# Kernel optimization log

Hardware: AMD Instinct MI355X
Metric: run time of the kernel (lower is better)

Reference implementation:

```python
import jax, jax.numpy as jnp
import numpy as np
from jax import lax

CODEBOOK_DIM = 32
SCALE_SCHEDULE = [1, 2, 4, 8, 16, 32, 64, 128, 256, 512, 1024, 2048, 4096, 8192]
INV_TEMP = 100.0
COMMIT_W = 0.2
ENTROPY_W = 0.1
EPS_NORM = 1e-12
EPS_LOG = 1e-8


def setup_inputs() -> dict:
    key = jax.random.key(0)
    B, T, C = 32, 8192, CODEBOOK_DIM
    f_BTC = jax.random.normal(key, (B, T, C), dtype=jnp.float32)
    return {"f_BTC": f_BTC}


def _area_down(x, pt):
    # torch F.interpolate mode='area' on divisible sizes == average pooling
    B, T, C = x.shape
    if pt == T:
        return x
    return x.reshape(B, pt, T // pt, C).mean(axis=2)


def _linear_up(x, out_size):
    # torch F.interpolate mode='linear', align_corners=False
    B, in_size, C = x.shape
    if out_size == in_size:
        return x
    scale = in_size / out_size
    pos = (jnp.arange(out_size, dtype=jnp.float32) + 0.5) * scale - 0.5
    pos = jnp.clip(pos, 0.0, in_size - 1)
    lo = jnp.floor(pos).astype(jnp.int32)
    hi = jnp.minimum(lo + 1, in_size - 1)
    w = (pos - lo.astype(jnp.float32))[None, :, None]
    return x[:, lo] * (1.0 - w) + x[:, hi] * w


def _bsq_level(z):
    # normalize
    norm = jnp.sqrt(jnp.sum(z * z, axis=-1, keepdims=True))
    z = z / jnp.maximum(norm, EPS_NORM)
    q_scale = 1.0 / (CODEBOOK_DIM ** 0.5)
    zhat = jnp.where(z > 0, q_scale, -q_scale).astype(z.dtype)
    quant = z + lax.stop_gradient(zhat - z)  # STE
    # soft entropy loss
    p = jax.nn.sigmoid(-4.0 * z / (CODEBOOK_DIM ** 0.5) * INV_TEMP)
    ent = lambda c: -(c * jnp.log(c + EPS_LOG))
    per_sample = (ent(p) + ent(1.0 - p)).sum(axis=-1).mean()
    avg_p = p.mean(axis=(0, 1))  # [C]
    cb_ent = (ent(avg_p) + ent(1.0 - avg_p)).sum()
    entropy_penalty = (per_sample - cb_ent) / INV_TEMP
    commit = jnp.mean(((lax.stop_gradient(quant) - z) ** 2).sum(axis=-1))
    aux = entropy_penalty * ENTROPY_W + commit * COMMIT_W
    bits = (quant > 0).astype(jnp.int32)
    return quant, bits, aux


def reference(f_BTC):
    B, T, C = f_BTC.shape
    quantized_out = jnp.zeros_like(f_BTC)
    residual = f_BTC
    all_losses, all_bits = [], []
    for pt in SCALE_SCHEDULE:
        r = _area_down(residual, pt)
        quant, bits, loss = _bsq_level(r)
        q_up = _linear_up(quant, T)
        residual = residual - lax.stop_gradient(q_up)
        quantized_out = quantized_out + q_up
        all_bits.append(bits)
        all_losses.append(loss)
    return quantized_out, jnp.concatenate(all_bits, axis=1), jnp.stack(all_losses, axis=-1)
```

## Files before the change

### kernel.cpp

```cpp
#include <hip/hip_runtime.h>

#define B_DIM 32
#define T_DIM 8192
#define C_DIM 32
#define N_ELEM (B_DIM * T_DIM * C_DIM)
#define SUM_PT 16383
#define BITS_ELEM (B_DIM * SUM_PT * C_DIM)
#define NLEVEL 14
#define PARTB 8192
#define PARTS 512
#define QSCALE 0.17677669529663687f
#define ALPHA  70.710678118654755f

#define OWN 128
#define HALO 16
#define MAXL (OWN + 2 * HALO)

__device__ __forceinline__ float entf(float x) { return -(x * __logf(x + 1e-8f)); }
__device__ __forceinline__ float qval(float bit) { return bit * (2.0f * QSCALE) - QSCALE; }

__device__ __forceinline__ float interp_pk(const unsigned int* __restrict__ pkbase,
                                           int ptj, float tpos, int c) {
    const float a = (float)ptj * (1.0f / (float)T_DIM);
    float pos = (tpos + 0.5f) * a - 0.5f;
    pos = fminf(fmaxf(pos, 0.0f), (float)(ptj - 1));
    const int lo = (int)pos;
    const int hi = min(lo + 1, ptj - 1);
    const float w = pos - (float)lo;
    const float b0 = (float)((pkbase[lo] >> c) & 1u);
    const float b1 = (float)((pkbase[hi] >> c) & 1u);
    return ((b0 * (1.0f - w) + b1 * w) * 2.0f - 1.0f) * QSCALE;
}

template <int PTJ>
__device__ __forceinline__ float interp_loc(const unsigned int* __restrict__ bl,
                                            int p0, float tpos, int c) {
    const float a = (float)PTJ * (1.0f / (float)T_DIM);
    float pos = (tpos + 0.5f) * a - 0.5f;
    pos = fminf(fmaxf(pos, 0.0f), (float)(PTJ - 1));
    const int lo = (int)pos;
    const int hi = min(lo + 1, PTJ - 1);
    const float w = pos - (float)lo;
    const float b0 = (float)((bl[lo - p0] >> c) & 1u);
    const float b1 = (float)((bl[hi - p0] >> c) & 1u);
    return ((b0 * (1.0f - w) + b1 * w) * 2.0f - 1.0f) * QSCALE;
}

__device__ __forceinline__ float evalT(const unsigned int* __restrict__ bl,
                                       float w, int pk, int c) {
    const float b0 = (float)((bl[pk & 0xFFFF] >> c) & 1u);
    const float b1 = (float)((bl[pk >> 16] >> c) & 1u);
    return ((b0 * (1.0f - w) + b1 * w) * 2.0f - 1.0f) * QSCALE;
}

__device__ float pooled_up_sum64(const float* base, int ptj, int m) {
    const int W = 64;
    const float a = (float)ptj * (1.0f / (float)T_DIM);
    const float p0 = ((float)(m * W) + 0.5f) * a - 0.5f;
    const float pmax = (float)(ptj - 1);
    float sum = 0.0f;
    int iL = 0;
    if (p0 < 0.0f) { iL = (int)ceilf(-p0 / a); if (iL > W) iL = W; }
    int iH = W - 1;
    if (p0 + (float)(W - 1) * a > pmax) {
        iH = (int)floorf((pmax - p0) / a);
        if (iH > W - 1) iH = W - 1;
        if (iH < -1) iH = -1;
    }
    if (iL > 0) sum += (float)iL * qval(base[0]);
    if (iH < W - 1) sum += (float)(W - 1 - iH) * qval(base[(size_t)(ptj - 1) * C_DIM]);
    if (iH >= iL) {
        const float pL = p0 + (float)iL * a;
        int l0 = (int)pL;
        if (l0 > ptj - 1) l0 = ptj - 1;
        const int is = (int)ceilf(((float)(l0 + 1) - p0) / a);
        const int endA = min(is - 1, iH);
        if (endA >= iL) {
            const int nA = endA - iL + 1;
            const float sI = 0.5f * (float)(iL + endA) * (float)nA;
            const float SA = (float)nA * (p0 - (float)l0) + a * sI;
            const float q0 = qval(base[(size_t)l0 * C_DIM]);
            const float q1 = qval(base[(size_t)min(l0 + 1, ptj - 1) * C_DIM]);
            sum += (float)nA * q0 + SA * (q1 - q0);
        }
        const int begB = max(is, iL);
        if (begB <= iH) {
            const int nB = iH - begB + 1;
            const float sI = 0.5f * (float)(begB + iH) * (float)nB;
            const float SB = (float)nB * (p0 - (float)(l0 + 1)) + a * sI;
            const float q1 = qval(base[(size_t)min(l0 + 1, ptj - 1) * C_DIM]);
            const float q2 = qval(base[(size_t)min(l0 + 2, ptj - 1) * C_DIM]);
            sum += (float)nB * q1 + SB * (q2 - q1);
        }
    }
    return sum;
}

__device__ __forceinline__ void wave_partials(float e, float cm, float p,
                                              float* base, int stride, int col) {
    float eg = e, cg = cm;
#pragma unroll
    for (int m = 32; m >= 1; m >>= 1) { eg += __shfl_xor(eg, m, 64); cg += __shfl_xor(cg, m, 64); }
    const float p2 = p + __shfl_xor(p, 32, 64);
    const int lane = threadIdx.x & 63;
    if (lane < 32) base[(size_t)(2 + lane) * stride + col] = p2;
    if (lane == 0) { base[col] = eg; base[(size_t)stride + col] = cg; }
}

__device__ __forceinline__ float bsq_eval(float v, float& bit, float& pA, float& eA, float& cA) {
    float sq = v * v;
#pragma unroll
    for (int m = 16; m >= 1; m >>= 1) sq += __shfl_xor(sq, m, 32);
    const float z = v / fmaxf(sqrtf(sq), 1e-12f);
    bit = (z > 0.f) ? 1.0f : 0.0f;
    const float zh = (z > 0.f) ? QSCALE : -QSCALE;
    const float d = zh - z;
    cA += d * d;
    const float p = 1.0f / (1.0f + __expf(ALPHA * z));
    pA += p;
    eA += entf(p) + entf(1.0f - p);
    return zh;
}

__global__ void init_kernel(const float* __restrict__ f, float* __restrict__ F128) {
    const int b = blockIdx.x >> 7, m = blockIdx.x & 127;
    const int c = threadIdx.x & 31, grp = threadIdx.x >> 5;
    const float* fb = f + ((size_t)b * T_DIM + m * 64 + grp * 8) * C_DIM + c;
    float s = 0.f;
#pragma unroll
    for (int i = 0; i < 8; ++i) s += fb[i * C_DIM];
    __shared__ float red[8][32];
    red[grp][c] = s;
    __syncthreads();
    if (grp == 0) {
        float t = red[0][c] + red[1][c] + red[2][c] + red[3][c]
                + red[4][c] + red[5][c] + red[6][c] + red[7][c];
        F128[((size_t)b * 128 + m) * C_DIM + c] = t * (1.0f / 64.0f);
    }
}

__global__ __launch_bounds__(1024) void fused_small_kernel(const float* __restrict__ F128,
                                                           float* __restrict__ bits,
                                                           unsigned int* __restrict__ pkG,
                                                           float* __restrict__ pSm) {
    const int b = blockIdx.x;
    __shared__ float P[128 * 32];
    __shared__ float qh[127 * 32];
    const int c = threadIdx.x & 31, grp = threadIdx.x >> 5;
    const int col = b * 16 + (threadIdx.x >> 6);
    for (int i = threadIdx.x; i < 128 * 32; i += 1024) P[i] = F128[(size_t)b * 128 * 32 + i];
    __syncthreads();
    for (int k = 0; k < 8; ++k) {
        const int pt = 1 << k, W2 = 128 >> k;
        float pAcc = 0.f, eAcc = 0.f, cAcc = 0.f;
        for (int o = grp; o < pt; o += 32) {
            float v = 0.f;
            for (int i = 0; i < W2; ++i) v += P[(o * W2 + i) * 32 + c];
            v *= (1.0f / (float)W2);
            float bit;
            bsq_eval(v, bit, pAcc, eAcc, cAcc);
            bits[((size_t)b * SUM_PT + (pt - 1) + o) * C_DIM + c] = bit;
            const unsigned long long bal = __ballot(bit > 0.5f);
            if (c == 0)
                pkG[(size_t)b * 256 + (pt - 1) + o] =
                    (threadIdx.x & 32) ? (unsigned)(bal >> 32) : (unsigned)bal;
            if (k < 7) qh[((pt - 1) + o) * 32 + c] = bit;
        }
        wave_partials(eAcc, cAcc, pAcc, pSm + (size_t)k * 34 * PARTS, PARTS, col);
        if (k < 7) {
            __syncthreads();
            for (int m = grp; m < 128; m += 32)
                P[m * 32 + c] -= pooled_up_sum64(&qh[(pt - 1) * 32 + c], 1 << k, m) * (1.0f / 64.0f);
            __syncthreads();
        }
    }
}

template <int K, int J, int TO>
__device__ __forceinline__ void buildTab(float* tw, int* ti, int L0, int nL) {
    constexpr int FK = 4096 >> K;
    constexpr int ptj = 1 << J;
    constexpr int FJ = 4096 >> J;
    const int pN = nL / FK;
    const int p0j = L0 / FJ;
    const int pNj = nL / FJ;
    for (int pl = threadIdx.x; pl < pN; pl += 512) {
        const float tpos = (float)(2 * (L0 + pl * FK) + FK) - 0.5f;
        const float a = (float)ptj * (1.0f / (float)T_DIM);
        float pos = (tpos + 0.5f) * a - 0.5f;
        pos = fminf(fmaxf(pos, 0.0f), (float)(ptj - 1));
        const int lo = (int)pos;
        const int hi = min(lo + 1, ptj - 1);
        tw[TO + pl] = pos - (float)lo;
        const int lol = min(max(lo - p0j, 0), pNj - 1);
        const int hil = min(max(hi - p0j, 0), pNj - 1);
        ti[TO + pl] = lol | (hil << 16);
    }
}

template <int K>
__device__ __forceinline__ void cf_level(const float* Rl, unsigned int* bitsPyr,
                                         const float* tw, const int* ti,
                                         float* __restrict__ bits,
                                         float* __restrict__ pBig,
                                         int b, int L0, int nL, int r0, int r1,
                                         int c, int grp, int col) {
    constexpr int F = 4096 >> K;
    constexpr int ptk = 1 << K;
    constexpr int OFF = (K == 8) ? 0 : (K == 9) ? 10 : (K == 10) ? 30 : (K == 11) ? 70 : 150;
    constexpr int TB8 = (K == 9) ? 0 : (K == 10) ? 20 : (K == 11) ? 100 : 340;
    constexpr int TB9 = (K == 10) ? 60 : (K == 11) ? 180 : 500;
    constexpr int TB10 = (K == 11) ? 260 : 660;
    constexpr int TB11 = 820;
    const int p0 = L0 / F, pN = nL / F;
    const int own0 = r0 / F, own1 = r1 / F;
    unsigned int* bl = bitsPyr + OFF;
    float pAcc = 0.f, eAcc = 0.f, cAcc = 0.f;
    for (int pl = grp; pl < pN; pl += 16) {
        float v = 0.f;
#pragma unroll
        for (int r = 0; r < F; ++r) v += Rl[(pl * F + r) * 32 + c];
        v *= (1.0f / (float)F);
        if (K >= 9)  v -= evalT(bitsPyr + 0,  tw[TB8 + pl],  ti[TB8 + pl], c);
        if (K >= 10) v -= evalT(bitsPyr + 10, tw[TB9 + pl],  ti[TB9 + pl], c);
        if (K >= 11) v -= evalT(bitsPyr + 30, tw[TB10 + pl], ti[TB10 + pl], c);
        if (K >= 12) v -= evalT(bitsPyr + 70, tw[TB11 + pl], ti[TB11 + pl], c);
        float sq = v * v;
#pragma unroll
        for (int m = 16; m >= 1; m >>= 1) sq += __shfl_xor(sq, m, 32);
        const float z = v / fmaxf(sqrtf(sq), 1e-12f);
        const unsigned long long bal = __ballot(z > 0.f);
        const unsigned int word = (threadIdx.x & 32) ? (unsigned)(bal >> 32) : (unsigned)bal;
        if (c == 0) bl[pl] = word;
        const int mg = p0 + pl;
        if (mg >= own0 && mg < own1) {
            bits[((size_t)b * SUM_PT + (ptk - 1) + mg) * C_DIM + c] = (z > 0.f) ? 1.f : 0.f;
            const float zh = (z > 0.f) ? QSCALE : -QSCALE;
            const float d = zh - z;
            cAcc += d * d;
            const float p = 1.0f / (1.0f + __expf(ALPHA * z));
            pAcc += p;
            eAcc += entf(p) + entf(1.0f - p);
        }
    }
    wave_partials(eAcc, cAcc, pAcc, pBig + (size_t)(K - 8) * 34 * PARTB, PARTB, col);
    __syncthreads();
}

__global__ __launch_bounds__(512) void chunk_final_kernel(const float* __restrict__ f,
                                                          float* __restrict__ outQ,
                                                          float* __restrict__ bits,
                                                          const unsigned int* __restrict__ pkG,
                                                          float* __restrict__ pBig) {
    const int b = blockIdx.x >> 5;
    const int chunk = blockIdx.x & 31;
    const int r0 = chunk * OWN, r1 = r0 + OWN;
    const int L0 = max(0, r0 - HALO);
    const int L1 = min(4096, r1 + HALO);
    const int nL = L1 - L0;
    const int nSeg = nL >> 4;
    __shared__ float Rl[MAXL * 32];
    __shared__ unsigned int bitsPyr[310];
    __shared__ unsigned int pk07[255];
    __shared__ float segA[16][32], segB[16][32];
    __shared__ float tw[980];
    __shared__ int ti[980];
    const int c = threadIdx.x & 31, grp = threadIdx.x >> 5;
    const int col = blockIdx.x * 8 + (threadIdx.x >> 6);

    const float* fb = f + ((size_t)b * T_DIM + (size_t)L0 * 2) * C_DIM;
    for (int i = threadIdx.x; i < nL * 8; i += 512) {
        const int row = i >> 3, c4 = i & 7;
        const float4 v0 = *(const float4*)(fb + (size_t)(2 * row) * 32 + c4 * 4);
        const float4 v1 = *(const float4*)(fb + (size_t)(2 * row + 1) * 32 + c4 * 4);
        float4 o;
        o.x = 0.5f * (v0.x + v1.x); o.y = 0.5f * (v0.y + v1.y);
        o.z = 0.5f * (v0.z + v1.z); o.w = 0.5f * (v0.w + v1.w);
        *(float4*)(Rl + row * 32 + c4 * 4) = o;
    }
    for (int i = threadIdx.x; i < 255; i += 512) pk07[i] = pkG[(size_t)b * 256 + i];
    buildTab<9, 8, 0>(tw, ti, L0, nL);
    buildTab<10, 8, 20>(tw, ti, L0, nL);
    buildTab<10, 9, 60>(tw, ti, L0, nL);
    buildTab<11, 8, 100>(tw, ti, L0, nL);
    buildTab<11, 9, 180>(tw, ti, L0, nL);
    buildTab<11, 10, 260>(tw, ti, L0, nL);
    buildTab<12, 8, 340>(tw, ti, L0, nL);
    buildTab<12, 9, 500>(tw, ti, L0, nL);
    buildTab<12, 10, 660>(tw, ti, L0, nL);
    buildTab<12, 11, 820>(tw, ti, L0, nL);
    __syncthreads();

    for (int w = threadIdx.x; w < nSeg * 32; w += 512) {
        const int s = w >> 5, cc = w & 31;
        const int rg = L0 + s * 16;
        float c0 = 0.f, c1 = 0.f;
#pragma unroll
        for (int j = 0; j < 8; ++j) {
            const int ptj = 1 << j;
            c0 += interp_pk(pk07 + (ptj - 1), ptj, (float)(2 * rg) + 0.5f, cc);
            c1 += interp_pk(pk07 + (ptj - 1), ptj, (float)(2 * rg + 2) + 0.5f, cc);
        }
        segA[s][cc] = c0;
        segB[s][cc] = c1 - c0;
    }
    __syncthreads();
    for (int rl = grp; rl < nL; rl += 16) {
        const int s = rl >> 4;
        Rl[rl * 32 + c] -= fmaf((float)(rl & 15), segB[s][c], segA[s][c]);
    }
    __syncthreads();

    cf_level<8>(Rl, bitsPyr, tw, ti, bits, pBig, b, L0, nL, r0, r1, c, grp, col);
    cf_level<9>(Rl, bitsPyr, tw, ti, bits, pBig, b, L0, nL, r0, r1, c, grp, col);
    cf_level<10>(Rl, bitsPyr, tw, ti, bits, pBig, b, L0, nL, r0, r1, c, grp, col);
    cf_level<11>(Rl, bitsPyr, tw, ti, bits, pBig, b, L0, nL, r0, r1, c, grp, col);
    cf_level<12>(Rl, bitsPyr, tw, ti, bits, pBig, b, L0, nL, r0, r1, c, grp, col);

    const int t0 = 2 * r0;
    const int p8 = L0 / 16, p9 = L0 / 8, p10 = L0 / 4, p11 = L0 / 2;
    for (int w = threadIdx.x; w < 16 * 32; w += 512) {
        const int s = w >> 5, cc = w & 31;
        const int tA = t0 + s * 16;
        float c0 = 0.f, c1 = 0.f;
#pragma unroll
        for (int j = 0; j < 8; ++j) {
            const int ptj = 1 << j;
            c0 += interp_pk(pk07 + (ptj - 1), ptj, (float)tA, cc);
            c1 += interp_pk(pk07 + (ptj - 1), ptj, (float)(tA + 1), cc);
        }
        c0 += interp_loc<256>(bitsPyr + 0, p8, (float)tA, cc);
        c1 += interp_loc<256>(bitsPyr + 0, p8, (float)(tA + 1), cc);
        segA[s][cc] = c0;
        segB[s][cc] = c1 - c0;
    }
    __syncthreads();
    const unsigned int* bl9 = bitsPyr + 10;
    const unsigned int* bl10 = bitsPyr + 30;
    const unsigned int* bl11 = bitsPyr + 70;
    const unsigned int* bl12 = bitsPyr + 150;
    float pAcc = 0.f, eAcc = 0.f, cAcc = 0.f;
    for (int j2 = grp; j2 < OWN; j2 += 16) {
        const int mg = r0 + j2;
        const int lr = mg - L0;
        const int te = 2 * mg;
        const int tte = 2 * j2;
        const int s = tte >> 4;

        const int e9 = te & 15;
        int lo9 = (te >> 4) - 1 + (e9 >= 8 ? 1 : 0);
        float w9e = (e9 < 8 ? (float)(17 + 2 * e9) : (float)(2 * e9 - 15)) * (1.0f / 32.0f);
        float w9o = w9e + (1.0f / 16.0f);
        if (lo9 < 0) { lo9 = 0; w9e = 0.f; w9o = 0.f; }
        const int hi9 = min(lo9 + 1, 511);
        const float b9a = (float)((bl9[lo9 - p9] >> c) & 1u);
        const float b9b = (float)((bl9[hi9 - p9] >> c) & 1u);

        const int e10 = te & 7;
        int lo10 = (te >> 3) - 1 + (e10 >= 4 ? 1 : 0);
        float w10e = (e10 < 4 ? (float)(9 + 2 * e10) : (float)(2 * e10 - 7)) * (1.0f / 16.0f);
        float w10o = w10e + (1.0f / 8.0f);
        if (lo10 < 0) { lo10 = 0; w10e = 0.f; w10o = 0.f; }
        const int hi10 = min(lo10 + 1, 1023);
        const float b10a = (float)((bl10[lo10 - p10] >> c) & 1u);
        const float b10b = (float)((bl10[hi10 - p10] >> c) & 1u);

        const int e11 = te & 3;
        int lo11 = (te >> 2) - 1 + (e11 >= 2 ? 1 : 0);
        float w11e = (e11 < 2 ? (float)(5 + 2 * e11) : (float)(2 * e11 - 3)) * (1.0f / 8.0f);
        float w11o = w11e + (1.0f / 4.0f);
        if (lo11 < 0) { lo11 = 0; w11e = 0.f; w11o = 0.f; }
        const int hi11 = min(lo11 + 1, 2047);
        const float b11a = (float)((bl11[lo11 - p11] >> c) & 1u);
        const float b11b = (float)((bl11[hi11 - p11] >> c) & 1u);

        const float q12m1 = (float)((bl12[max(lr - 1, 0)] >> c) & 1u);
        const float q12z = (float)((bl12[lr] >> c) & 1u);
        const float q12p1 = (float)((bl12[min(lr + 1, nL - 1)] >> c) & 1u);
        const float w12e = (mg == 0) ? 0.f : 0.75f;
        const float w12o = 0.25f;

        float upe = fmaf((float)(tte & 15), segB[s][c], segA[s][c]);
        upe += ((b9a * (1.0f - w9e) + b9b * w9e) * 2.0f - 1.0f) * QSCALE;
        upe += ((b10a * (1.0f - w10e) + b10b * w10e) * 2.0f - 1.0f) * QSCALE;
        upe += ((b11a * (1.0f - w11e) + b11b * w11e) * 2.0f - 1.0f) * QSCALE;
        upe += ((q12m1 * (1.0f - w12e) + q12z * w12e) * 2.0f - 1.0f) * QSCALE;

        float upo = fmaf((float)((tte + 1) & 15), segB[s][c], segA[s][c]);
        upo += ((b9a * (1.0f - w9o) + b9b * w9o) * 2.0f - 1.0f) * QSCALE;
        upo += ((b10a * (1.0f - w10o) + b10b * w10o) * 2.0f - 1.0f) * QSCALE;
        upo += ((b11a * (1.0f - w11o) + b11b * w11o) * 2.0f - 1.0f) * QSCALE;
        upo += ((q12z * (1.0f - w12o) + q12p1 * w12o) * 2.0f - 1.0f) * QSCALE;

        {
            const size_t idx = ((size_t)b * T_DIM + te) * C_DIM + c;
            const float v = f[idx] - upe;
            float bit;
            const float zh = bsq_eval(v, bit, pAcc, eAcc, cAcc);
            bits[((size_t)b * SUM_PT + (T_DIM - 1) + te) * C_DIM + c] = bit;
            outQ[idx] = upe + zh;
        }
        {
            const size_t idx = ((size_t)b * T_DIM + te + 1) * C_DIM + c;
            const float v = f[idx] - upo;
            float bit;
            const float zh = bsq_eval(v, bit, pAcc, eAcc, cAcc);
            bits[((size_t)b * SUM_PT + (T_DIM - 1) + te + 1) * C_DIM + c] = bit;
            outQ[idx] = upo + zh;
        }
    }
    wave_partials(eAcc, cAcc, pAcc, pBig + (size_t)5 * 34 * PARTB, PARTB, col);
}

__global__ void reduce_partials(const float* __restrict__ pSm,
                                const float* __restrict__ pBig,
                                float* __restrict__ acc) {
    const int level = blockIdx.x / 34;
    const int comp = blockIdx.x % 34;
    const float* s;
    int n;
    if (level < 8) { s = pSm + ((size_t)level * 34 + comp) * PARTS; n = PARTS; }
    else { s = pBig + ((size_t)(level - 8) * 34 + comp) * PARTB; n = PARTB; }
    float v = 0.f;
    for (int i = threadIdx.x; i < n; i += 64) v += s[i];
#pragma unroll
    for (int m = 32; m >= 1; m >>= 1) v += __shfl_xor(v, m, 64);
    if (threadIdx.x == 0) acc[level * 34 + comp] = v;
}

__global__ void finalize_kernel(const float* __restrict__ acc, float* __restrict__ outL) {
    const int k = threadIdx.x >> 5;
    const int c = threadIdx.x & 31;
    if (k >= NLEVEL) return;
    const float cnt = (float)(B_DIM << k);
    const float avg_p = acc[k * 34 + 2 + c] / cnt;
    float ec = entf(avg_p) + entf(1.0f - avg_p);
#pragma unroll
    for (int m = 16; m >= 1; m >>= 1) ec += __shfl_xor(ec, m, 32);
    if (c == 0) {
        const float per_sample = acc[k * 34 + 0] / cnt;
        const float commit = acc[k * 34 + 1] / cnt;
        const float pen = (per_sample - ec) * (1.0f / 100.0f);
        outL[k] = pen * 0.1f + commit * 0.2f;
    }
}

extern "C" void kernel_launch(void* const* d_in, const int* in_sizes, int n_in,
                              void* d_out, int out_size, void* d_ws, size_t ws_size,
                              hipStream_t stream) {
    (void)in_sizes; (void)n_in; (void)out_size; (void)ws_size;
    const float* f = (const float*)d_in[0];
    float* outQ = (float*)d_out;
    float* outBits = outQ + N_ELEM;
    float* outL = outBits + BITS_ELEM;

    float* pSm = (float*)d_ws;
    float* pBig = pSm + (size_t)8 * 34 * PARTS;
    float* acc = pBig + (size_t)6 * 34 * PARTB;
    float* F128 = acc + NLEVEL * 34;
    unsigned int* pkG = (unsigned int*)(F128 + (size_t)B_DIM * 128 * C_DIM);

    init_kernel<<<B_DIM * 128, 256, 0, stream>>>(f, F128);
    fused_small_kernel<<<B_DIM, 1024, 0, stream>>>(F128, outBits, pkG, pSm);
    chunk_final_kernel<<<B_DIM * 32, 512, 0, stream>>>(f, outQ, outBits, pkG, pBig);
    reduce_partials<<<NLEVEL * 34, 64, 0, stream>>>(pSm, pBig, acc);
    finalize_kernel<<<1, 512, 0, stream>>>(acc, outL);
}
```

Baseline: 173.9 us.

## Fuse coarse-level pyramid into chunk kernel with redundant per-block recompute

Removes the separate 32-block fused_small_kernel and instead has every chunk block recompute the coarse levels 0-7 from F128 in shared memory, with only chunk 0 writing bits and partials. This drops a low-occupancy serial kernel launch and the pkG global round trip. In exchange each of 1024 blocks repeats the small-level work, and shared memory is unioned so the two phases share one buffer. PARTS is halved to match the 8 waves per block.

```diff
diff --git a/kernel.cpp b/kernel.cpp
--- a/kernel.cpp
+++ b/kernel.cpp
@@ -8,7 +8,7 @@
 #define BITS_ELEM (B_DIM * SUM_PT * C_DIM)
 #define NLEVEL 14
 #define PARTB 8192
-#define PARTS 512
+#define PARTS 256
 #define QSCALE 0.17677669529663687f
 #define ALPHA  70.710678118654755f
 
@@ -120,60 +120,6 @@
     pA += p;
     eA += entf(p) + entf(1.0f - p);
     return zh;
-}
-
-__global__ void init_kernel(const float* __restrict__ f, float* __restrict__ F128) {
-    const int b = blockIdx.x >> 7, m = blockIdx.x & 127;
-    const int c = threadIdx.x & 31, grp = threadIdx.x >> 5;
-    const float* fb = f + ((size_t)b * T_DIM + m * 64 + grp * 8) * C_DIM + c;
-    float s = 0.f;
-#pragma unroll
-    for (int i = 0; i < 8; ++i) s += fb[i * C_DIM];
-    __shared__ float red[8][32];
-    red[grp][c] = s;
-    __syncthreads();
-    if (grp == 0) {
-        float t = red[0][c] + red[1][c] + red[2][c] + red[3][c]
-                + red[4][c] + red[5][c] + red[6][c] + red[7][c];
-        F128[((size_t)b * 128 + m) * C_DIM + c] = t * (1.0f / 64.0f);
-    }
-}
-
-__global__ __launch_bounds__(1024) void fused_small_kernel(const float* __restrict__ F128,
-                                                           float* __restrict__ bits,
-                                                           unsigned int* __restrict__ pkG,
-                                                           float* __restrict__ pSm) {
-    const int b = blockIdx.x;
-    __shared__ float P[128 * 32];
-    __shared__ float qh[127 * 32];
-    const int c = threadIdx.x & 31, grp = threadIdx.x >> 5;
-    const int col = b * 16 + (threadIdx.x >> 6);
-    for (int i = threadIdx.x; i < 128 * 32; i += 1024) P[i] = F128[(size_t)b * 128 * 32 + i];
-    __syncthreads();
-    for (int k = 0; k < 8; ++k) {
-        const int pt = 1 << k, W2 = 128 >> k;
-        float pAcc = 0.f, eAcc = 0.f, cAcc = 0.f;
-        for (int o = grp; o < pt; o += 32) {
-            float v = 0.f;
-            for (int i = 0; i < W2; ++i) v += P[(o * W2 + i) * 32 + c];
-            v *= (1.0f / (float)W2);
-            float bit;
-            bsq_eval(v, bit, pAcc, eAcc, cAcc);
-            bits[((size_t)b * SUM_PT + (pt - 1) + o) * C_DIM + c] = bit;
-            const unsigned long long bal = __ballot(bit > 0.5f);
-            if (c == 0)
-                pkG[(size_t)b * 256 + (pt - 1) + o] =
-                    (threadIdx.x & 32) ? (unsigned)(bal >> 32) : (unsigned)bal;
-            if (k < 7) qh[((pt - 1) + o) * 32 + c] = bit;
-        }
-        wave_partials(eAcc, cAcc, pAcc, pSm + (size_t)k * 34 * PARTS, PARTS, col);
-        if (k < 7) {
-            __syncthreads();
-            for (int m = grp; m < 128; m += 32)
-                P[m * 32 + c] -= pooled_up_sum64(&qh[(pt - 1) * 32 + c], 1 << k, m) * (1.0f / 64.0f);
-            __syncthreads();
-        }
-    }
 }
 
 template <int K, int J, int TO>
@@ -247,11 +193,29 @@
     __syncthreads();
 }
 
-__global__ __launch_bounds__(512) void chunk_final_kernel(const float* __restrict__ f,
-                                                          float* __restrict__ outQ,
-                                                          float* __restrict__ bits,
-                                                          const unsigned int* __restrict__ pkG,
-                                                          float* __restrict__ pBig) {
+__global__ void init_kernel(const float* __restrict__ f, float* __restrict__ F128) {
+    const int b = blockIdx.x >> 7, m = blockIdx.x & 127;
+    const int c = threadIdx.x & 31, grp = threadIdx.x >> 5;
+    const float* fb = f + ((size_t)b * T_DIM + m * 64 + grp * 8) * C_DIM + c;
+    float s = 0.f;
+#pragma unroll
+    for (int i = 0; i < 8; ++i) s += fb[i * C_DIM];
+    __shared__ float red[8][32];
+    red[grp][c] = s;
+    __syncthreads();
+    if (grp == 0) {
+        float t = red[0][c] + red[1][c] + red[2][c] + red[3][c]
+                + red[4][c] + red[5][c] + red[6][c] + red[7][c];
+        F128[((size_t)b * 128 + m) * C_DIM + c] = t * (1.0f / 64.0f);
+    }
+}
+
+__global__ __launch_bounds__(512) void chunk_kernel(const float* __restrict__ f,
+                                                    float* __restrict__ outQ,
+                                                    float* __restrict__ bits,
+                                                    const float* __restrict__ F128,
+                                                    float* __restrict__ pSm,
+                                                    float* __restrict__ pBig) {
     const int b = blockIdx.x >> 5;
     const int chunk = blockIdx.x & 31;
     const int r0 = chunk * OWN, r1 = r0 + OWN;
@@ -259,26 +223,61 @@
     const int L1 = min(4096, r1 + HALO);
     const int nL = L1 - L0;
     const int nSeg = nL >> 4;
-    __shared__ float Rl[MAXL * 32];
-    __shared__ unsigned int bitsPyr[310];
+    __shared__ __align__(16) char uni[33712];
     __shared__ unsigned int pk07[255];
-    __shared__ float segA[16][32], segB[16][32];
-    __shared__ float tw[980];
-    __shared__ int ti[980];
+    float* Rl = (float*)uni;
+    unsigned int* bitsPyr = (unsigned int*)(uni + 20480);
+    float (*segA)[32] = (float(*)[32])(uni + 21760);
+    float (*segB)[32] = (float(*)[32])(uni + 23808);
+    float* tw = (float*)(uni + 25856);
+    int* ti = (int*)(uni + 29776);
+    float* Pb = (float*)uni;
+    float* qh = (float*)(uni + 16384);
     const int c = threadIdx.x & 31, grp = threadIdx.x >> 5;
-    const int col = blockIdx.x * 8 + (threadIdx.x >> 6);
-
-    const float* fb = f + ((size_t)b * T_DIM + (size_t)L0 * 2) * C_DIM;
-    for (int i = threadIdx.x; i < nL * 8; i += 512) {
-        const int row = i >> 3, c4 = i & 7;
-        const float4 v0 = *(const float4*)(fb + (size_t)(2 * row) * 32 + c4 * 4);
-        const float4 v1 = *(const float4*)(fb + (size_t)(2 * row + 1) * 32 + c4 * 4);
-        float4 o;
-        o.x = 0.5f * (v0.x + v1.x); o.y = 0.5f * (v0.y + v1.y);
-        o.z = 0.5f * (v0.z + v1.z); o.w = 0.5f * (v0.w + v1.w);
-        *(float4*)(Rl + row * 32 + c4 * 4) = o;
-    }
-    for (int i = threadIdx.x; i < 255; i += 512) pk07[i] = pkG[(size_t)b * 256 + i];
+    const int wave = threadIdx.x >> 6;
+    const int col = blockIdx.x * 8 + wave;
+    const bool wr0 = (chunk == 0);
+
+    for (int i = threadIdx.x; i < 128 * 32; i += 512) Pb[i] = F128[(size_t)b * 4096 + i];
+    __syncthreads();
+    for (int k = 0; k < 8; ++k) {
+        const int pt = 1 << k, W2 = 128 >> k;
+        float pAcc = 0.f, eAcc = 0.f, cAcc = 0.f;
+        for (int o = grp; o < pt; o += 16) {
+            float v = 0.f;
+            for (int i = 0; i < W2; ++i) v += Pb[(o * W2 + i) * 32 + c];
+            v *= (1.0f / (float)W2);
+            float bit;
+            bsq_eval(v, bit, pAcc, eAcc, cAcc);
+            if (wr0) bits[((size_t)b * SUM_PT + (pt - 1) + o) * C_DIM + c] = bit;
+            const unsigned long long bal = __ballot(bit > 0.5f);
+            if (c == 0)
+                pk07[(pt - 1) + o] =
+                    (threadIdx.x & 32) ? (unsigned)(bal >> 32) : (unsigned)bal;
+            if (k < 7) qh[((pt - 1) + o) * 32 + c] = bit;
+        }
+        if (wr0) wave_partials(eAcc, cAcc, pAcc, pSm + (size_t)k * 34 * PARTS, PARTS, b * 8 + wave);
+        if (k < 7) {
+            __syncthreads();
+            for (int m = grp; m < 128; m += 16)
+                Pb[m * 32 + c] -= pooled_up_sum64(&qh[(pt - 1) * 32 + c], 1 << k, m) * (1.0f / 64.0f);
+            __syncthreads();
+        }
+    }
+    __syncthreads();
+
+    {
+        const float* fb = f + ((size_t)b * T_DIM + (size_t)L0 * 2) * C_DIM;
+        for (int i = threadIdx.x; i < nL * 8; i += 512) {
+            const int row = i >> 3, c4 = i & 7;
+            const float4 v0 = *(const float4*)(fb + (size_t)(2 * row) * 32 + c4 * 4);
+            const float4 v1 = *(const float4*)(fb + (size_t)(2 * row + 1) * 32 + c4 * 4);
+            float4 o;
+            o.x = 0.5f * (v0.x + v1.x); o.y = 0.5f * (v0.y + v1.y);
+            o.z = 0.5f * (v0.z + v1.z); o.w = 0.5f * (v0.w + v1.w);
+            *(float4*)(Rl + row * 32 + c4 * 4) = o;
+        }
+    }
     buildTab<9, 8, 0>(tw, ti, L0, nL);
     buildTab<10, 8, 20>(tw, ti, L0, nL);
     buildTab<10, 9, 60>(tw, ti, L0, nL);
@@ -317,99 +316,101 @@
     cf_level<11>(Rl, bitsPyr, tw, ti, bits, pBig, b, L0, nL, r0, r1, c, grp, col);
     cf_level<12>(Rl, bitsPyr, tw, ti, bits, pBig, b, L0, nL, r0, r1, c, grp, col);
 
-    const int t0 = 2 * r0;
-    const int p8 = L0 / 16, p9 = L0 / 8, p10 = L0 / 4, p11 = L0 / 2;
-    for (int w = threadIdx.x; w < 16 * 32; w += 512) {
-        const int s = w >> 5, cc = w & 31;
-        const int tA = t0 + s * 16;
-        float c0 = 0.f, c1 = 0.f;
-#pragma unroll
-        for (int j = 0; j < 8; ++j) {
-            const int ptj = 1 << j;
-            c0 += interp_pk(pk07 + (ptj - 1), ptj, (float)tA, cc);
-            c1 += interp_pk(pk07 + (ptj - 1), ptj, (float)(tA + 1), cc);
-        }
-        c0 += interp_loc<256>(bitsPyr + 0, p8, (float)tA, cc);
-        c1 += interp_loc<256>(bitsPyr + 0, p8, (float)(tA + 1), cc);
-        segA[s][cc] = c0;
-        segB[s][cc] = c1 - c0;
-    }
-    __syncthreads();
-    const unsigned int* bl9 = bitsPyr + 10;
-    const unsigned int* bl10 = bitsPyr + 30;
-    const unsigned int* bl11 = bitsPyr + 70;
-    const unsigned int* bl12 = bitsPyr + 150;
-    float pAcc = 0.f, eAcc = 0.f, cAcc = 0.f;
-    for (int j2 = grp; j2 < OWN; j2 += 16) {
-        const int mg = r0 + j2;
-        const int lr = mg - L0;
-        const int te = 2 * mg;
-        const int tte = 2 * j2;
-        const int s = tte >> 4;
-
-        const int e9 = te & 15;
-        int lo9 = (te >> 4) - 1 + (e9 >= 8 ? 1 : 0);
-        float w9e = (e9 < 8 ? (float)(17 + 2 * e9) : (float)(2 * e9 - 15)) * (1.0f / 32.0f);
-        float w9o = w9e + (1.0f / 16.0f);
-        if (lo9 < 0) { lo9 = 0; w9e = 0.f; w9o = 0.f; }
-        const int hi9 = min(lo9 + 1, 511);
-        const float b9a = (float)((bl9[lo9 - p9] >> c) & 1u);
-        const float b9b = (float)((bl9[hi9 - p9] >> c) & 1u);
-
-        const int e10 = te & 7;
-        int lo10 = (te >> 3) - 1 + (e10 >= 4 ? 1 : 0);
-        float w10e = (e10 < 4 ? (float)(9 + 2 * e10) : (float)(2 * e10 - 7)) * (1.0f / 16.0f);
-        float w10o = w10e + (1.0f / 8.0f);
-        if (lo10 < 0) { lo10 = 0; w10e = 0.f; w10o = 0.f; }
-        const int hi10 = min(lo10 + 1, 1023);
-        const float b10a = (float)((bl10[lo10 - p10] >> c) & 1u);
-        const float b10b = (float)((bl10[hi10 - p10] >> c) & 1u);
-
-        const int e11 = te & 3;
-        int lo11 = (te >> 2) - 1 + (e11 >= 2 ? 1 : 0);
-        float w11e = (e11 < 2 ? (float)(5 + 2 * e11) : (float)(2 * e11 - 3)) * (1.0f / 8.0f);
-        float w11o = w11e + (1.0f / 4.0f);
-        if (lo11 < 0) { lo11 = 0; w11e = 0.f; w11o = 0.f; }
-        const int hi11 = min(lo11 + 1, 2047);
-        const float b11a = (float)((bl11[lo11 - p11] >> c) & 1u);
-        const float b11b = (float)((bl11[hi11 - p11] >> c) & 1u);
-
-        const float q12m1 = (float)((bl12[max(lr - 1, 0)] >> c) & 1u);
-        const float q12z = (float)((bl12[lr] >> c) & 1u);
-        const float q12p1 = (float)((bl12[min(lr + 1, nL - 1)] >> c) & 1u);
-        const float w12e = (mg == 0) ? 0.f : 0.75f;
-        const float w12o = 0.25f;
-
-        float upe = fmaf((float)(tte & 15), segB[s][c], segA[s][c]);
-        upe += ((b9a * (1.0f - w9e) + b9b * w9e) * 2.0f - 1.0f) * QSCALE;
-        upe += ((b10a * (1.0f - w10e) + b10b * w10e) * 2.0f - 1.0f) * QSCALE;
-        upe += ((b11a * (1.0f - w11e) + b11b * w11e) * 2.0f - 1.0f) * QSCALE;
-        upe += ((q12m1 * (1.0f - w12e) + q12z * w12e) * 2.0f - 1.0f) * QSCALE;
-
-        float upo = fmaf((float)((tte + 1) & 15), segB[s][c], segA[s][c]);
-        upo += ((b9a * (1.0f - w9o) + b9b * w9o) * 2.0f - 1.0f) * QSCALE;
-        upo += ((b10a * (1.0f - w10o) + b10b * w10o) * 2.0f - 1.0f) * QSCALE;
-        upo += ((b11a * (1.0f - w11o) + b11b * w11o) * 2.0f - 1.0f) * QSCALE;
-        upo += ((q12z * (1.0f - w12o) + q12p1 * w12o) * 2.0f - 1.0f) * QSCALE;
-
-        {
-            const size_t idx = ((size_t)b * T_DIM + te) * C_DIM + c;
-            const float v = f[idx] - upe;
-            float bit;
-            const float zh = bsq_eval(v, bit, pAcc, eAcc, cAcc);
-            bits[((size_t)b * SUM_PT + (T_DIM - 1) + te) * C_DIM + c] = bit;
-            outQ[idx] = upe + zh;
-        }
-        {
-            const size_t idx = ((size_t)b * T_DIM + te + 1) * C_DIM + c;
-            const float v = f[idx] - upo;
-            float bit;
-            const float zh = bsq_eval(v, bit, pAcc, eAcc, cAcc);
-            bits[((size_t)b * SUM_PT + (T_DIM - 1) + te + 1) * C_DIM + c] = bit;
-            outQ[idx] = upo + zh;
-        }
-    }
-    wave_partials(eAcc, cAcc, pAcc, pBig + (size_t)5 * 34 * PARTB, PARTB, col);
+    {
+        const int t0 = 2 * r0;
+        const int p8 = L0 / 16, p9 = L0 / 8, p10 = L0 / 4, p11 = L0 / 2;
+        for (int w = threadIdx.x; w < 16 * 32; w += 512) {
+            const int s = w >> 5, cc = w & 31;
+            const int tA = t0 + s * 16;
+            float c0 = 0.f, c1 = 0.f;
+#pragma unroll
+            for (int j = 0; j < 8; ++j) {
+                const int ptj = 1 << j;
+                c0 += interp_pk(pk07 + (ptj - 1), ptj, (float)tA, cc);
+                c1 += interp_pk(pk07 + (ptj - 1), ptj, (float)(tA + 1), cc);
+            }
+            c0 += interp_loc<256>(bitsPyr + 0, p8, (float)tA, cc);
+            c1 += interp_loc<256>(bitsPyr + 0, p8, (float)(tA + 1), cc);
+            segA[s][cc] = c0;
+            segB[s][cc] = c1 - c0;
+        }
+        __syncthreads();
+        const unsigned int* bl9 = bitsPyr + 10;
+        const unsigned int* bl10 = bitsPyr + 30;
+        const unsigned int* bl11 = bitsPyr + 70;
+        const unsigned int* bl12 = bitsPyr + 150;
+        float pAcc = 0.f, eAcc = 0.f, cAcc = 0.f;
+        for (int j2 = grp; j2 < OWN; j2 += 16) {
+            const int mg = r0 + j2;
+            const int lr = mg - L0;
+            const int te = 2 * mg;
+            const int tte = 2 * j2;
+            const int s = tte >> 4;
+
+            const int e9 = te & 15;
+            int lo9 = (te >> 4) - 1 + (e9 >= 8 ? 1 : 0);
+            float w9e = (e9 < 8 ? (float)(17 + 2 * e9) : (float)(2 * e9 - 15)) * (1.0f / 32.0f);
+            float w9o = w9e + (1.0f / 16.0f);
+            if (lo9 < 0) { lo9 = 0; w9e = 0.f; w9o = 0.f; }
+            const int hi9 = min(lo9 + 1, 511);
+            const float b9a = (float)((bl9[lo9 - p9] >> c) & 1u);
+            const float b9b = (float)((bl9[hi9 - p9] >> c) & 1u);
+
+            const int e10 = te & 7;
+            int lo10 = (te >> 3) - 1 + (e10 >= 4 ? 1 : 0);
+            float w10e = (e10 < 4 ? (float)(9 + 2 * e10) : (float)(2 * e10 - 7)) * (1.0f / 16.0f);
+            float w10o = w10e + (1.0f / 8.0f);
+            if (lo10 < 0) { lo10 = 0; w10e = 0.f; w10o = 0.f; }
+            const int hi10 = min(lo10 + 1, 1023);
+            const float b10a = (float)((bl10[lo10 - p10] >> c) & 1u);
+            const float b10b = (float)((bl10[hi10 - p10] >> c) & 1u);
+
+            const int e11 = te & 3;
+            int lo11 = (te >> 2) - 1 + (e11 >= 2 ? 1 : 0);
+            float w11e = (e11 < 2 ? (float)(5 + 2 * e11) : (float)(2 * e11 - 3)) * (1.0f / 8.0f);
+            float w11o = w11e + (1.0f / 4.0f);
+            if (lo11 < 0) { lo11 = 0; w11e = 0.f; w11o = 0.f; }
+            const int hi11 = min(lo11 + 1, 2047);
+            const float b11a = (float)((bl11[lo11 - p11] >> c) & 1u);
+            const float b11b = (float)((bl11[hi11 - p11] >> c) & 1u);
+
+            const float q12m1 = (float)((bl12[max(lr - 1, 0)] >> c) & 1u);
+            const float q12z = (float)((bl12[lr] >> c) & 1u);
+            const float q12p1 = (float)((bl12[min(lr + 1, nL - 1)] >> c) & 1u);
+            const float w12e = (mg == 0) ? 0.f : 0.75f;
+            const float w12o = 0.25f;
+
+            float upe = fmaf((float)(tte & 15), segB[s][c], segA[s][c]);
+            upe += ((b9a * (1.0f - w9e) + b9b * w9e) * 2.0f - 1.0f) * QSCALE;
+            upe += ((b10a * (1.0f - w10e) + b10b * w10e) * 2.0f - 1.0f) * QSCALE;
+            upe += ((b11a * (1.0f - w11e) + b11b * w11e) * 2.0f - 1.0f) * QSCALE;
+            upe += ((q12m1 * (1.0f - w12e) + q12z * w12e) * 2.0f - 1.0f) * QSCALE;
+
+            float upo = fmaf((float)((tte + 1) & 15), segB[s][c], segA[s][c]);
+            upo += ((b9a * (1.0f - w9o) + b9b * w9o) * 2.0f - 1.0f) * QSCALE;
+            upo += ((b10a * (1.0f - w10o) + b10b * w10o) * 2.0f - 1.0f) * QSCALE;
+            upo += ((b11a * (1.0f - w11o) + b11b * w11o) * 2.0f - 1.0f) * QSCALE;
+            upo += ((q12z * (1.0f - w12o) + q12p1 * w12o) * 2.0f - 1.0f) * QSCALE;
+
+            {
+                const size_t idx = ((size_t)b * T_DIM + te) * C_DIM + c;
+                const float v = f[idx] - upe;
+                float bit;
+                const float zh = bsq_eval(v, bit, pAcc, eAcc, cAcc);
+                bits[((size_t)b * SUM_PT + (T_DIM - 1) + te) * C_DIM + c] = bit;
+                outQ[idx] = upe + zh;
+            }
+            {
+                const size_t idx = ((size_t)b * T_DIM + te + 1) * C_DIM + c;
+                const float v = f[idx] - upo;
+                float bit;
+                const float zh = bsq_eval(v, bit, pAcc, eAcc, cAcc);
+                bits[((size_t)b * SUM_PT + (T_DIM - 1) + te + 1) * C_DIM + c] = bit;
+                outQ[idx] = upo + zh;
+            }
+        }
+        wave_partials(eAcc, cAcc, pAcc, pBig + (size_t)5 * 34 * PARTB, PARTB, col);
+    }
 }
 
 __global__ void reduce_partials(const float* __restrict__ pSm,
@@ -458,11 +459,9 @@
     float* pBig = pSm + (size_t)8 * 34 * PARTS;
     float* acc = pBig + (size_t)6 * 34 * PARTB;
     float* F128 = acc + NLEVEL * 34;
-    unsigned int* pkG = (unsigned int*)(F128 + (size_t)B_DIM * 128 * C_DIM);
 
     init_kernel<<<B_DIM * 128, 256, 0, stream>>>(f, F128);
-    fused_small_kernel<<<B_DIM, 1024, 0, stream>>>(F128, outBits, pkG, pSm);
-    chunk_final_kernel<<<B_DIM * 32, 512, 0, stream>>>(f, outQ, outBits, pkG, pBig);
+    chunk_kernel<<<B_DIM * 32, 512, 0, stream>>>(f, outQ, outBits, F128, pSm, pBig);
     reduce_partials<<<NLEVEL * 34, 64, 0, stream>>>(pSm, pBig, acc);
     finalize_kernel<<<1, 512, 0, stream>>>(acc, outL);
 }
```

Result: slower. 220.2 us (+26.6%).
